# Performance work log

Hardware: AMD Instinct MI355X
Metric: run time of the kernel (lower is better)

Reference implementation:

```python
import jax, jax.numpy as jnp
import numpy as np

N_NODES = 100_000
N_EDGES = 1_600_000
N_GRAPHS = 512
D_IN = 128
D_H = 64
D_OUT = 32
N_CONV = 4  # n_layers - 1
BN_EPS = 1e-5


def setup_inputs() -> dict:
    key = jax.random.key(0)
    ks = jax.random.split(key, 10)
    h = jax.random.normal(ks[0], (N_NODES, D_IN), dtype=jnp.float32)
    src = jax.random.randint(ks[1], (N_EDGES,), 0, N_NODES, dtype=jnp.int32)
    dst = jax.random.randint(ks[2], (N_EDGES,), 0, N_NODES, dtype=jnp.int32)
    graph_ids = jnp.sort(jax.random.randint(ks[3], (N_NODES,), 0, N_GRAPHS, dtype=jnp.int32))
    s = 0.05
    fc1_w0 = jax.random.normal(ks[4], (D_IN, D_H), dtype=jnp.float32) * s
    fc1_w = jax.random.normal(ks[5], (N_CONV - 1, D_H, D_H), dtype=jnp.float32) * s
    fc2_w = jax.random.normal(ks[6], (N_CONV, D_H, D_H), dtype=jnp.float32) * s
    bn1_g = jnp.ones((N_CONV, D_H), dtype=jnp.float32)
    bn1_b = jnp.zeros((N_CONV, D_H), dtype=jnp.float32)
    bn2_g = jnp.ones((N_CONV, D_H), dtype=jnp.float32)
    bn2_b = jnp.zeros((N_CONV, D_H), dtype=jnp.float32)
    pred_w = jax.random.normal(ks[7], (N_CONV, D_H, D_OUT), dtype=jnp.float32) * s
    pred_b = jnp.zeros((N_CONV, D_OUT), dtype=jnp.float32)
    return {"h": h, "src": src, "dst": dst, "graph_ids": graph_ids,
            "fc1_w0": fc1_w0, "fc1_w": fc1_w, "fc2_w": fc2_w,
            "bn1_g": bn1_g, "bn1_b": bn1_b, "bn2_g": bn2_g, "bn2_b": bn2_b,
            "pred_w": pred_w, "pred_b": pred_b}


def _batch_norm(x, g, b):
    # PyTorch training-mode BN: batch mean, biased variance
    m = jnp.mean(x, axis=0)
    v = jnp.var(x, axis=0)
    return (x - m) * jax.lax.rsqrt(v + BN_EPS) * g + b


def reference(h, src, dst, graph_ids, fc1_w0, fc1_w, fc2_w,
              bn1_g, bn1_b, bn2_g, bn2_b, pred_w, pred_b):
    # GIN: h' = MLP((1+eps)*h + sum_{j in N(i)} h_j), eps=0 (learn_eps=False)
    score = jnp.zeros((N_GRAPHS, D_OUT), dtype=h.dtype)
    for l in range(N_CONV):
        agg = h + jax.ops.segment_sum(h[src], dst, num_segments=N_NODES)
        w1 = fc1_w0 if l == 0 else fc1_w[l - 1]
        # _MLP: fc2(relu(BN(fc1(x))))
        h = jax.nn.relu(_batch_norm(agg @ w1, bn1_g[l], bn1_b[l])) @ fc2_w[l]
        # outer BN + relu
        h = jax.nn.relu(_batch_norm(h, bn2_g[l], bn2_b[l]))
        # SumPooling per graph; readout skips layer-0 input rep, dropout is eval-mode identity
        pooled = jax.ops.segment_sum(h, graph_ids, num_segments=N_GRAPHS)
        score = score + pooled @ pred_w[l] + pred_b[l]
    return score
```

## Files before the change

### kernel.cpp

```cpp
#include <hip/hip_runtime.h>

#define N_NODES 100000
#define N_EDGES 1600000
#define N_GRAPHS 512
#define D_IN 128
#define D_H 64
#define D_OUT 32
#define N_CONV 4
#define BN_EPS 1e-5f
#define NSLOT 32

#define NB 512
#define NPB 196
#define NBUSED 511
#define CHUNK 8192
#define MAXE 4096
#define AGG_BLOCKS 2048
#define AGG_CHUNKS 3125

typedef unsigned short ushort_t;
typedef unsigned int uint_t;
typedef __attribute__((ext_vector_type(8))) short bf16x8;
typedef __attribute__((ext_vector_type(4))) float f32x4;
union U4B8 { uint4 u; bf16x8 v; };

__device__ inline float b2f(ushort_t u) {
    union { uint_t i; float f; } c; c.i = ((uint_t)u) << 16; return c.f;
}
__device__ inline ushort_t f2b(float f) {
    union { uint_t i; float f; } c; c.f = f;
    uint_t r = (c.i + 0x7fffu + ((c.i >> 16) & 1u)) >> 16;
    return (ushort_t)r;
}
__device__ inline float blo(uint_t v) { return b2f((ushort_t)(v & 0xffffu)); }
__device__ inline float bhi(uint_t v) { return b2f((ushort_t)(v >> 16)); }

__global__ __launch_bounds__(256) void zero_kernel(int* __restrict__ p, int nwords) {
    int i = blockIdx.x * 256 + threadIdx.x;
    if (i < nwords) p[i] = 0;
}

__global__ __launch_bounds__(256) void bucket_count(const int* __restrict__ dst,
                                                    int* __restrict__ bucketCnt) {
    __shared__ int l[NB];
    int t = threadIdx.x;
    for (int i = t; i < NB; i += 256) l[i] = 0;
    __syncthreads();
    long base = (long)blockIdx.x * 4096;
    for (int i = t; i < 4096; i += 256) {
        long e = base + i;
        if (e < N_EDGES) atomicAdd(&l[(unsigned)dst[e] / NPB], 1);
    }
    __syncthreads();
    for (int i = t; i < NB; i += 256) if (l[i]) atomicAdd(&bucketCnt[i], l[i]);
}

__global__ __launch_bounds__(512) void bucket_scan(const int* __restrict__ bucketCnt,
                                                   int* __restrict__ bucketOffs,
                                                   int* __restrict__ bucketCur) {
    __shared__ int s[512];
    int t = threadIdx.x;
    int v = bucketCnt[t];
    s[t] = v;
    __syncthreads();
    for (int off = 1; off < 512; off <<= 1) {
        int u = (t >= off) ? s[t - off] : 0;
        __syncthreads();
        s[t] += u;
        __syncthreads();
    }
    int excl = s[t] - v;
    bucketOffs[t] = excl;
    bucketCur[t] = excl;
    if (t == 511) bucketOffs[512] = s[511];
}

__global__ __launch_bounds__(256) void binned_scatter(const int* __restrict__ src,
                                                      const int* __restrict__ dst,
                                                      int* __restrict__ bucketCur,
                                                      uint_t* __restrict__ pairs) {
    __shared__ uint_t sortedp[CHUNK];
    __shared__ ushort_t sbkt[CHUNK];
    __shared__ int lcnt[NB], loffs[NB], lcur[NB], gbase[NB];
    __shared__ int ps[256];
    int t = threadIdx.x;
    long e0 = (long)blockIdx.x * CHUNK;
    int nvalid = (int)min((long)CHUNK, (long)N_EDGES - e0);
    for (int i = t; i < NB; i += 256) lcnt[i] = 0;
    __syncthreads();
    for (int i = t; i < nvalid; i += 256)
        atomicAdd(&lcnt[(unsigned)dst[e0 + i] / NPB], 1);
    __syncthreads();
    int a0 = lcnt[2 * t], a1 = lcnt[2 * t + 1];
    ps[t] = a0 + a1;
    __syncthreads();
    for (int off = 1; off < 256; off <<= 1) {
        int u = (t >= off) ? ps[t - off] : 0;
        __syncthreads();
        ps[t] += u;
        __syncthreads();
    }
    int ex = ps[t] - (a0 + a1);
    loffs[2 * t] = ex; loffs[2 * t + 1] = ex + a0;
    lcur[2 * t] = ex;  lcur[2 * t + 1] = ex + a0;
    __syncthreads();
    for (int i = t; i < NB; i += 256) {
        int c = lcnt[i];
        gbase[i] = c ? atomicAdd(&bucketCur[i], c) : 0;
    }
    for (int i = t; i < nvalid; i += 256) {
        int d = dst[e0 + i];
        int b = (unsigned)d / NPB;
        int pos = atomicAdd(&lcur[b], 1);
        sortedp[pos] = ((uint_t)src[e0 + i] << 9) | (uint_t)(d - b * NPB);
        sbkt[pos] = (ushort_t)b;
    }
    __syncthreads();
    for (int i = t; i < nvalid; i += 256) {
        int b = sbkt[i];
        long gpos = (long)gbase[b] + (i - loffs[b]);
        pairs[gpos] = sortedp[i];
    }
}

__global__ __launch_bounds__(256) void csr_finalize(const uint_t* __restrict__ pairs,
                                                    const int* __restrict__ bucketOffs,
                                                    int* __restrict__ offs,
                                                    int* __restrict__ csr) {
    __shared__ uint_t lp[MAXE];
    __shared__ int lsrc[MAXE];
    __shared__ int lcnt[NPB], lcur[NPB];
    __shared__ int ls[256];
    int b = blockIdx.x, t = threadIdx.x;
    int e0 = bucketOffs[b], e1 = bucketOffs[b + 1];
    int ne = e1 - e0;
    int n0 = b * NPB;
    int nn = min(NPB, N_NODES - n0);
    for (int i = t; i < ne; i += 256) lp[i] = pairs[e0 + i];
    for (int i = t; i < nn; i += 256) lcnt[i] = 0;
    __syncthreads();
    for (int i = t; i < ne; i += 256) atomicAdd(&lcnt[lp[i] & 511u], 1);
    __syncthreads();
    int v = (t < nn) ? lcnt[t] : 0;
    ls[t] = v;
    __syncthreads();
    for (int off = 1; off < 256; off <<= 1) {
        int u = (t >= off) ? ls[t - off] : 0;
        __syncthreads();
        ls[t] += u;
        __syncthreads();
    }
    if (t < nn) { lcur[t] = ls[t] - v; offs[n0 + t] = e0 + ls[t] - v; }
    if (t == 0 && b == NBUSED - 1) offs[N_NODES] = e1;
    __syncthreads();
    for (int i = t; i < ne; i += 256) {
        uint_t p = lp[i];
        int pos = atomicAdd(&lcur[p & 511u], 1);
        lsrc[pos] = (int)(p >> 9);
    }
    __syncthreads();
    for (int i = t; i < ne; i += 256) csr[e0 + i] = lsrc[i];
}

#define SLABS 4
#define GEMM_BLOCKS 391
__global__ __launch_bounds__(256) void gemm0(const float* __restrict__ in,
                                             const float* __restrict__ w,
                                             ushort_t* __restrict__ y16) {
    __shared__ uint4 Bl[4][4][64];
    int t = threadIdx.x;
    for (int idx = t; idx < 4 * 4 * 64; idx += 256) {
        int l = idx & 63, nt = (idx >> 6) & 3, kk = idx >> 8;
        int k0 = kk * 32 + ((l >> 4) << 3), c = nt * 16 + (l & 15);
        uint4 o;
        o.x = (uint_t)f2b(w[(k0 + 0) * 64 + c]) | ((uint_t)f2b(w[(k0 + 1) * 64 + c]) << 16);
        o.y = (uint_t)f2b(w[(k0 + 2) * 64 + c]) | ((uint_t)f2b(w[(k0 + 3) * 64 + c]) << 16);
        o.z = (uint_t)f2b(w[(k0 + 4) * 64 + c]) | ((uint_t)f2b(w[(k0 + 5) * 64 + c]) << 16);
        o.w = (uint_t)f2b(w[(k0 + 6) * 64 + c]) | ((uint_t)f2b(w[(k0 + 7) * 64 + c]) << 16);
        Bl[kk][nt][l] = o;
    }
    __syncthreads();
    int wv = t >> 6, lane = t & 63, lq = lane >> 4, lr = lane & 15;
    bf16x8 B[4][4];
#pragma unroll
    for (int kk = 0; kk < 4; kk++)
#pragma unroll
        for (int nt = 0; nt < 4; nt++) { U4B8 cv; cv.u = Bl[kk][nt][lane]; B[kk][nt] = cv.v; }
    for (int s = 0; s < SLABS; s++) {
        long rb = ((long)blockIdx.x * SLABS + s) * 64 + wv * 16;
        long n = rb + lr;
        const float* rp = in + (n < N_NODES ? n : 0) * 128;
        f32x4 zero = {0.f, 0.f, 0.f, 0.f};
        f32x4 acc[4] = {zero, zero, zero, zero};
#pragma unroll
        for (int kk = 0; kk < 4; kk++) {
            float4 u = *(const float4*)(rp + kk * 32 + lq * 8);
            float4 v = *(const float4*)(rp + kk * 32 + lq * 8 + 4);
            bf16x8 a;
            a[0] = (short)f2b(u.x); a[1] = (short)f2b(u.y);
            a[2] = (short)f2b(u.z); a[3] = (short)f2b(u.w);
            a[4] = (short)f2b(v.x); a[5] = (short)f2b(v.y);
            a[6] = (short)f2b(v.z); a[7] = (short)f2b(v.w);
#pragma unroll
            for (int nt = 0; nt < 4; nt++)
                acc[nt] = __builtin_amdgcn_mfma_f32_16x16x32_bf16(a, B[kk][nt], acc[nt], 0, 0, 0);
        }
#pragma unroll
        for (int nt = 0; nt < 4; nt++)
#pragma unroll
            for (int j = 0; j < 4; j++) {
                long rr = rb + lq * 4 + j;
                if (rr < N_NODES) y16[rr * 64 + nt * 16 + lr] = f2b(acc[nt][j]);
            }
    }
}

template <bool OSTAT>
__global__ __launch_bounds__(256) void gemm_bn(const uint4* __restrict__ in,
                                               const float* __restrict__ w,
                                               const float* __restrict__ bnip,
                                               const float* __restrict__ gi,
                                               const float* __restrict__ bi,
                                               ushort_t* __restrict__ outY,
                                               float* __restrict__ ostat) {
    __shared__ uint4 Bl[2][4][64];
    __shared__ float sc[64], sh[64];
    __shared__ float red1[4][64], red2[4][64];
    int t = threadIdx.x;
    if (t < 64) {
        float S = 0.f, S2 = 0.f;
        for (int s = 0; s < NSLOT; s++) { S += bnip[s * 128 + t]; S2 += bnip[s * 128 + 64 + t]; }
        float mean = S * (1.f / N_NODES);
        float var = S2 * (1.f / N_NODES) - mean * mean;
        float r = rsqrtf(var + BN_EPS);
        float scv = gi[t] * r;
        sc[t] = scv; sh[t] = bi[t] - mean * scv;
    }
    for (int idx = t; idx < 2 * 4 * 64; idx += 256) {
        int l = idx & 63, nt = (idx >> 6) & 3, kk = idx >> 8;
        int k0 = kk * 32 + ((l >> 4) << 3), c = nt * 16 + (l & 15);
        uint4 o;
        o.x = (uint_t)f2b(w[(k0 + 0) * 64 + c]) | ((uint_t)f2b(w[(k0 + 1) * 64 + c]) << 16);
        o.y = (uint_t)f2b(w[(k0 + 2) * 64 + c]) | ((uint_t)f2b(w[(k0 + 3) * 64 + c]) << 16);
        o.z = (uint_t)f2b(w[(k0 + 4) * 64 + c]) | ((uint_t)f2b(w[(k0 + 5) * 64 + c]) << 16);
        o.w = (uint_t)f2b(w[(k0 + 6) * 64 + c]) | ((uint_t)f2b(w[(k0 + 7) * 64 + c]) << 16);
        Bl[kk][nt][l] = o;
    }
    __syncthreads();
    int wv = t >> 6, lane = t & 63, lq = lane >> 4, lr = lane & 15;
    bf16x8 B[2][4];
#pragma unroll
    for (int kk = 0; kk < 2; kk++)
#pragma unroll
        for (int nt = 0; nt < 4; nt++) { U4B8 cv; cv.u = Bl[kk][nt][lane]; B[kk][nt] = cv.v; }
    float s1[4] = {0.f, 0.f, 0.f, 0.f}, s2[4] = {0.f, 0.f, 0.f, 0.f};
    for (int s = 0; s < SLABS; s++) {
        long rb = ((long)blockIdx.x * SLABS + s) * 64 + wv * 16;
        long n = rb + lr;
        bool ok = n < N_NODES;
        const uint4* rp = in + (ok ? n : 0) * 8;
        f32x4 zero = {0.f, 0.f, 0.f, 0.f};
        f32x4 acc[4] = {zero, zero, zero, zero};
#pragma unroll
        for (int kk = 0; kk < 2; kk++) {
            bf16x8 a;
            if (ok) {
                uint4 v = rp[kk * 4 + lq];
                int k0 = kk * 32 + lq * 8;
                float x0 = fmaxf(blo(v.x) * sc[k0 + 0] + sh[k0 + 0], 0.f);
                float x1 = fmaxf(bhi(v.x) * sc[k0 + 1] + sh[k0 + 1], 0.f);
                float x2 = fmaxf(blo(v.y) * sc[k0 + 2] + sh[k0 + 2], 0.f);
                float x3 = fmaxf(bhi(v.y) * sc[k0 + 3] + sh[k0 + 3], 0.f);
                float x4 = fmaxf(blo(v.z) * sc[k0 + 4] + sh[k0 + 4], 0.f);
                float x5 = fmaxf(bhi(v.z) * sc[k0 + 5] + sh[k0 + 5], 0.f);
                float x6 = fmaxf(blo(v.w) * sc[k0 + 6] + sh[k0 + 6], 0.f);
                float x7 = fmaxf(bhi(v.w) * sc[k0 + 7] + sh[k0 + 7], 0.f);
                a[0] = (short)f2b(x0); a[1] = (short)f2b(x1);
                a[2] = (short)f2b(x2); a[3] = (short)f2b(x3);
                a[4] = (short)f2b(x4); a[5] = (short)f2b(x5);
                a[6] = (short)f2b(x6); a[7] = (short)f2b(x7);
            } else {
#pragma unroll
                for (int j = 0; j < 8; j++) a[j] = 0;
            }
#pragma unroll
            for (int nt = 0; nt < 4; nt++)
                acc[nt] = __builtin_amdgcn_mfma_f32_16x16x32_bf16(a, B[kk][nt], acc[nt], 0, 0, 0);
        }
#pragma unroll
        for (int nt = 0; nt < 4; nt++)
#pragma unroll
            for (int j = 0; j < 4; j++) {
                long rr = rb + lq * 4 + j;
                float val = acc[nt][j];
                if (rr < N_NODES) outY[rr * 64 + nt * 16 + lr] = f2b(val);
                if (OSTAT) { s1[nt] += val; s2[nt] += val * val; }
            }
    }
    if (OSTAT) {
#pragma unroll
        for (int nt = 0; nt < 4; nt++) {
            s1[nt] += __shfl_xor(s1[nt], 16); s1[nt] += __shfl_xor(s1[nt], 32);
            s2[nt] += __shfl_xor(s2[nt], 16); s2[nt] += __shfl_xor(s2[nt], 32);
        }
        if (lq == 0) {
#pragma unroll
            for (int nt = 0; nt < 4; nt++) {
                red1[wv][nt * 16 + lr] = s1[nt];
                red2[wv][nt * 16 + lr] = s2[nt];
            }
        }
        __syncthreads();
        if (t < 64) {
            float S = red1[0][t] + red1[1][t] + red1[2][t] + red1[3][t];
            float S2 = red2[0][t] + red2[1][t] + red2[2][t] + red2[3][t];
            int slot = blockIdx.x & (NSLOT - 1);
            atomicAdd(&ostat[slot * 128 + t], S);
            atomicAdd(&ostat[slot * 128 + 64 + t], S2);
        }
    }
}

__global__ __launch_bounds__(256) void aggregate(const uint_t* __restrict__ y32,
                                                 const int* __restrict__ offs,
                                                 const int* __restrict__ csr,
                                                 uint_t* __restrict__ aggOut,
                                                 float* __restrict__ bn1p) {
    int t = threadIdx.x;
    int wv = t >> 6, lane = t & 63;
    int g = lane >> 3, l = lane & 7;
    __shared__ float l1[4][64], l2[4][64];
    float st1[8], st2[8];
#pragma unroll
    for (int m = 0; m < 8; m++) { st1[m] = 0.f; st2[m] = 0.f; }
    for (int chunk = blockIdx.x; chunk < AGG_CHUNKS; chunk += AGG_BLOCKS) {
        int nb_base = chunk * 32 + wv * 8;
        for (int j = 0; j < 8; j++) {
            int n = nb_base + j;
            int p0 = offs[n], p1 = offs[n + 1];
            int cnt = 1 + (p1 - p0);
            int rounds = (cnt + 7) >> 3;
            float accA[4] = {0.f, 0.f, 0.f, 0.f}, accB[4] = {0.f, 0.f, 0.f, 0.f};
            int e = g;
            int idx = (g == 0) ? n : ((g < cnt) ? csr[p0 + g - 1] : -1);
            uint4 v;
            if (idx >= 0) v = *(const uint4*)(y32 + (long)idx * 32 + 4 * l);
            for (int r = 0; r < rounds; r++) {
                int ne = e + 8;
                int nidx = (ne < cnt) ? csr[p0 + ne - 1] : -1;
                uint4 vn;
                if (nidx >= 0) vn = *(const uint4*)(y32 + (long)nidx * 32 + 4 * l);
                if (idx >= 0) {
                    accA[0] += __uint_as_float(v.x << 16);
                    accB[0] += __uint_as_float(v.x & 0xffff0000u);
                    accA[1] += __uint_as_float(v.y << 16);
                    accB[1] += __uint_as_float(v.y & 0xffff0000u);
                    accA[2] += __uint_as_float(v.z << 16);
                    accB[2] += __uint_as_float(v.z & 0xffff0000u);
                    accA[3] += __uint_as_float(v.w << 16);
                    accB[3] += __uint_as_float(v.w & 0xffff0000u);
                }
                e = ne; idx = nidx; v = vn;
            }
#pragma unroll
            for (int m = 0; m < 4; m++) {
                accA[m] += __shfl_xor(accA[m], 8);
                accB[m] += __shfl_xor(accB[m], 8);
                accA[m] += __shfl_xor(accA[m], 16);
                accB[m] += __shfl_xor(accB[m], 16);
                accA[m] += __shfl_xor(accA[m], 32);
                accB[m] += __shfl_xor(accB[m], 32);
            }
            if (g == 0) {
                uint4 o;
                o.x = (uint_t)f2b(accA[0]) | ((uint_t)f2b(accB[0]) << 16);
                o.y = (uint_t)f2b(accA[1]) | ((uint_t)f2b(accB[1]) << 16);
                o.z = (uint_t)f2b(accA[2]) | ((uint_t)f2b(accB[2]) << 16);
                o.w = (uint_t)f2b(accA[3]) | ((uint_t)f2b(accB[3]) << 16);
                *(uint4*)&aggOut[(long)n * 32 + 4 * l] = o;
                st1[0] += accA[0]; st2[0] += accA[0] * accA[0];
                st1[1] += accB[0]; st2[1] += accB[0] * accB[0];
                st1[2] += accA[1]; st2[2] += accA[1] * accA[1];
                st1[3] += accB[1]; st2[3] += accB[1] * accB[1];
                st1[4] += accA[2]; st2[4] += accA[2] * accA[2];
                st1[5] += accB[2]; st2[5] += accB[2] * accB[2];
                st1[6] += accA[3]; st2[6] += accA[3] * accA[3];
                st1[7] += accB[3]; st2[7] += accB[3] * accB[3];
            }
        }
    }
    if (g == 0) {
#pragma unroll
        for (int m = 0; m < 8; m++) { l1[wv][8 * l + m] = st1[m]; l2[wv][8 * l + m] = st2[m]; }
    }
    __syncthreads();
    if (t < 64) {
        float S = l1[0][t] + l1[1][t] + l1[2][t] + l1[3][t];
        float S2 = l2[0][t] + l2[1][t] + l2[2][t] + l2[3][t];
        int slot = blockIdx.x & (NSLOT - 1);
        atomicAdd(&bn1p[slot * 128 + t], S);
        atomicAdd(&bn1p[slot * 128 + 64 + t], S2);
    }
}

__global__ __launch_bounds__(256) void bn_pool(const uint_t* __restrict__ h2,
                                               const float* __restrict__ bn2p,
                                               const float* __restrict__ g2,
                                               const float* __restrict__ b2,
                                               const int* __restrict__ gid,
                                               float* __restrict__ pooled) {
    __shared__ float sc[64], sh[64];
    int t = threadIdx.x;
    if (t < 64) {
        float S = 0.f, S2 = 0.f;
        for (int s = 0; s < NSLOT; s++) { S += bn2p[s * 128 + t]; S2 += bn2p[s * 128 + 64 + t]; }
        float mean = S * (1.f / N_NODES);
        float var = S2 * (1.f / N_NODES) - mean * mean;
        float r = rsqrtf(var + BN_EPS);
        float scv = g2[t] * r;
        sc[t] = scv; sh[t] = b2[t] - mean * scv;
    }
    __syncthreads();
    int c = t & 31, rs = t >> 5;
    float sA = sc[2 * c], hA = sh[2 * c], sB = sc[2 * c + 1], hB = sh[2 * c + 1];
    long base = (long)blockIdx.x * 256;
    float pa = 0.f, pb2 = 0.f; int gc = -1;
    for (int i = 0; i < 32; i++) {
        long n = base + rs + 8 * i;
        if (n >= N_NODES) break;
        int g = gid[n];
        uint_t v = h2[n * 32 + c];
        float x0 = fmaxf(blo(v) * sA + hA, 0.f);
        float x1 = fmaxf(bhi(v) * sB + hB, 0.f);
        if (g != gc) {
            if (gc >= 0) {
                atomicAdd(&pooled[(long)gc * 64 + 2 * c], pa);
                atomicAdd(&pooled[(long)gc * 64 + 2 * c + 1], pb2);
            }
            gc = g; pa = 0.f; pb2 = 0.f;
        }
        pa += x0; pb2 += x1;
    }
    if (gc >= 0) {
        atomicAdd(&pooled[(long)gc * 64 + 2 * c], pa);
        atomicAdd(&pooled[(long)gc * 64 + 2 * c + 1], pb2);
    }
}

__global__ __launch_bounds__(256) void score_kernel(const float* __restrict__ pooled,
                                                    const float* __restrict__ pw,
                                                    const float* __restrict__ pb,
                                                    float* __restrict__ out) {
    int idx = blockIdx.x * 256 + threadIdx.x;
    int g = idx >> 5, o = idx & 31;
    float acc = 0.f;
    for (int l = 0; l < N_CONV; l++) {
        acc += pb[l * 32 + o];
        const float* pr = pooled + (long)l * N_GRAPHS * 64 + (long)g * 64;
        const float* wr = pw + l * 64 * 32;
        for (int k = 0; k < 64; k++) acc += pr[k] * wr[k * 32 + o];
    }
    out[idx] = acc;
}

extern "C" void kernel_launch(void* const* d_in, const int* in_sizes, int n_in,
                              void* d_out, int out_size, void* d_ws, size_t ws_size,
                              hipStream_t stream) {
    const float* h     = (const float*)d_in[0];
    const int*   src   = (const int*)d_in[1];
    const int*   dst   = (const int*)d_in[2];
    const int*   gid   = (const int*)d_in[3];
    const float* fc1w0 = (const float*)d_in[4];
    const float* fc1w  = (const float*)d_in[5];
    const float* fc2w  = (const float*)d_in[6];
    const float* bn1g  = (const float*)d_in[7];
    const float* bn1b  = (const float*)d_in[8];
    const float* bn2g  = (const float*)d_in[9];
    const float* bn2b  = (const float*)d_in[10];
    const float* pw    = (const float*)d_in[11];
    const float* pb    = (const float*)d_in[12];
    float* out = (float*)d_out;

    char* ws = (char*)d_ws;
    uint_t*   AGG16   = (uint_t*)  (ws);
    uint_t*   pairs   = (uint_t*)  (ws);
    ushort_t* X16     = (ushort_t*)(ws + 25600000);
    ushort_t* Y16     = (ushort_t*)(ws + 38400000);
    float*    bnst    = (float*)   (ws + 51200000);
    float*    pooled  = (float*)   (ws + 51331072);
    int*   bucketCnt  = (int*)     (ws + 51855360);
    int*   bucketOffs = (int*)     (ws + 51857408);
    int*   bucketCur  = (int*)     (ws + 51859460);
    int*   offs       = (int*)     (ws + 51861508);
    int*   csr        = (int*)     (ws + 52261512);

    const int zwords = (51857408 - 51200000) / 4;
    zero_kernel<<<(zwords + 255) / 256, 256, 0, stream>>>((int*)bnst, zwords);

    bucket_count<<<(N_EDGES + 4095) / 4096, 256, 0, stream>>>(dst, bucketCnt);
    bucket_scan<<<1, 512, 0, stream>>>(bucketCnt, bucketOffs, bucketCur);
    binned_scatter<<<(N_EDGES + CHUNK - 1) / CHUNK, 256, 0, stream>>>(src, dst, bucketCur, pairs);
    csr_finalize<<<NBUSED, 256, 0, stream>>>(pairs, bucketOffs, offs, csr);

    for (int l = 0; l < N_CONV; l++) {
        float* bn1p = bnst + (long)l * 8192;
        float* bn2p = bn1p + 4096;
        float* pl = pooled + (long)l * N_GRAPHS * 64;
        if (l == 0) {
            gemm0<<<GEMM_BLOCKS, 256, 0, stream>>>(h, fc1w0, Y16);
        } else {
            float* bn2p_prev = bnst + (long)(l - 1) * 8192 + 4096;
            gemm_bn<false><<<GEMM_BLOCKS, 256, 0, stream>>>((const uint4*)X16,
                fc1w + (long)(l - 1) * 4096, bn2p_prev,
                bn2g + (l - 1) * 64, bn2b + (l - 1) * 64, Y16, (float*)nullptr);
        }
        aggregate<<<AGG_BLOCKS, 256, 0, stream>>>((const uint_t*)Y16, offs, csr, AGG16, bn1p);
        gemm_bn<true><<<GEMM_BLOCKS, 256, 0, stream>>>((const uint4*)AGG16,
            fc2w + (long)l * 4096, bn1p, bn1g + l * 64, bn1b + l * 64, X16, bn2p);
        bn_pool<<<391, 256, 0, stream>>>((const uint_t*)X16, bn2p, bn2g + l * 64,
                                         bn2b + l * 64, gid, pl);
    }
    score_kernel<<<64, 256, 0, stream>>>(pooled, pw, pb, out);
}
```

Before: 405.7 us.

## Pipeline neighbor gathers via async global-to-LDS loads and shrink GEMM block work

The aggregate kernel now prefetches each node's first few neighbor rows straight into shared memory with global_load_lds, double-buffered two nodes ahead, and falls back to direct loads for high-degree nodes. This is meant to hide the gather latency that the old per-round register prefetch left exposed. The GEMM kernels also get more blocks with fewer row slabs each, for better occupancy. The cost is higher LDS use and hand-written waitcnt values that must match the number of outstanding loads.

Measured after the change: 420.9 us. 1.04x slower.

```diff
diff --git a/kernel.cpp b/kernel.cpp
--- a/kernel.cpp
+++ b/kernel.cpp
@@ -17,12 +17,16 @@
 #define MAXE 4096
 #define AGG_BLOCKS 2048
 #define AGG_CHUNKS 3125
+#define R_STAT 3
 
 typedef unsigned short ushort_t;
 typedef unsigned int uint_t;
 typedef __attribute__((ext_vector_type(8))) short bf16x8;
 typedef __attribute__((ext_vector_type(4))) float f32x4;
 union U4B8 { uint4 u; bf16x8 v; };
+
+typedef const __attribute__((address_space(1))) uint_t guint_t;
+typedef __attribute__((address_space(3))) uint_t luint_t;
 
 __device__ inline float b2f(ushort_t u) {
     union { uint_t i; float f; } c; c.i = ((uint_t)u) << 16; return c.f;
@@ -162,8 +166,9 @@
     for (int i = t; i < ne; i += 256) csr[e0 + i] = lsrc[i];
 }
 
-#define SLABS 4
-#define GEMM_BLOCKS 391
+#define G0_SLABS 2
+#define G0_BLOCKS 782
+#define GBN_BLOCKS 1563
 __global__ __launch_bounds__(256) void gemm0(const float* __restrict__ in,
                                              const float* __restrict__ w,
                                              ushort_t* __restrict__ y16) {
@@ -186,8 +191,8 @@
     for (int kk = 0; kk < 4; kk++)
 #pragma unroll
         for (int nt = 0; nt < 4; nt++) { U4B8 cv; cv.u = Bl[kk][nt][lane]; B[kk][nt] = cv.v; }
-    for (int s = 0; s < SLABS; s++) {
-        long rb = ((long)blockIdx.x * SLABS + s) * 64 + wv * 16;
+    for (int s = 0; s < G0_SLABS; s++) {
+        long rb = ((long)blockIdx.x * G0_SLABS + s) * 64 + wv * 16;
         long n = rb + lr;
         const float* rp = in + (n < N_NODES ? n : 0) * 128;
         f32x4 zero = {0.f, 0.f, 0.f, 0.f};
@@ -254,49 +259,48 @@
 #pragma unroll
         for (int nt = 0; nt < 4; nt++) { U4B8 cv; cv.u = Bl[kk][nt][lane]; B[kk][nt] = cv.v; }
     float s1[4] = {0.f, 0.f, 0.f, 0.f}, s2[4] = {0.f, 0.f, 0.f, 0.f};
-    for (int s = 0; s < SLABS; s++) {
-        long rb = ((long)blockIdx.x * SLABS + s) * 64 + wv * 16;
-        long n = rb + lr;
-        bool ok = n < N_NODES;
-        const uint4* rp = in + (ok ? n : 0) * 8;
-        f32x4 zero = {0.f, 0.f, 0.f, 0.f};
-        f32x4 acc[4] = {zero, zero, zero, zero};
-#pragma unroll
-        for (int kk = 0; kk < 2; kk++) {
-            bf16x8 a;
-            if (ok) {
-                uint4 v = rp[kk * 4 + lq];
-                int k0 = kk * 32 + lq * 8;
-                float x0 = fmaxf(blo(v.x) * sc[k0 + 0] + sh[k0 + 0], 0.f);
-                float x1 = fmaxf(bhi(v.x) * sc[k0 + 1] + sh[k0 + 1], 0.f);
-                float x2 = fmaxf(blo(v.y) * sc[k0 + 2] + sh[k0 + 2], 0.f);
-                float x3 = fmaxf(bhi(v.y) * sc[k0 + 3] + sh[k0 + 3], 0.f);
-                float x4 = fmaxf(blo(v.z) * sc[k0 + 4] + sh[k0 + 4], 0.f);
-                float x5 = fmaxf(bhi(v.z) * sc[k0 + 5] + sh[k0 + 5], 0.f);
-                float x6 = fmaxf(blo(v.w) * sc[k0 + 6] + sh[k0 + 6], 0.f);
-                float x7 = fmaxf(bhi(v.w) * sc[k0 + 7] + sh[k0 + 7], 0.f);
-                a[0] = (short)f2b(x0); a[1] = (short)f2b(x1);
-                a[2] = (short)f2b(x2); a[3] = (short)f2b(x3);
-                a[4] = (short)f2b(x4); a[5] = (short)f2b(x5);
-                a[6] = (short)f2b(x6); a[7] = (short)f2b(x7);
-            } else {
-#pragma unroll
-                for (int j = 0; j < 8; j++) a[j] = 0;
-            }
-#pragma unroll
-            for (int nt = 0; nt < 4; nt++)
-                acc[nt] = __builtin_amdgcn_mfma_f32_16x16x32_bf16(a, B[kk][nt], acc[nt], 0, 0, 0);
+    long rb = (long)blockIdx.x * 64 + wv * 16;
+    long n = rb + lr;
+    bool ok = n < N_NODES;
+    const uint4* rp = in + (ok ? n : 0) * 8;
+    f32x4 zero = {0.f, 0.f, 0.f, 0.f};
+    f32x4 acc[4] = {zero, zero, zero, zero};
+#pragma unroll
+    for (int kk = 0; kk < 2; kk++) {
+        bf16x8 a;
+        if (ok) {
+            uint4 v = rp[kk * 4 + lq];
+            int k0 = kk * 32 + lq * 8;
+            float x0 = fmaxf(blo(v.x) * sc[k0 + 0] + sh[k0 + 0], 0.f);
+            float x1 = fmaxf(bhi(v.x) * sc[k0 + 1] + sh[k0 + 1], 0.f);
+            float x2 = fmaxf(blo(v.y) * sc[k0 + 2] + sh[k0 + 2], 0.f);
+            float x3 = fmaxf(bhi(v.y) * sc[k0 + 3] + sh[k0 + 3], 0.f);
+            float x4 = fmaxf(blo(v.z) * sc[k0 + 4] + sh[k0 + 4], 0.f);
+            float x5 = fmaxf(bhi(v.z) * sc[k0 + 5] + sh[k0 + 5], 0.f);
+            float x6 = fmaxf(blo(v.w) * sc[k0 + 6] + sh[k0 + 6], 0.f);
+            float x7 = fmaxf(bhi(v.w) * sc[k0 + 7] + sh[k0 + 7], 0.f);
+            a[0] = (short)f2b(x0); a[1] = (short)f2b(x1);
+            a[2] = (short)f2b(x2); a[3] = (short)f2b(x3);
+            a[4] = (short)f2b(x4); a[5] = (short)f2b(x5);
+            a[6] = (short)f2b(x6); a[7] = (short)f2b(x7);
+        } else {
+#pragma unroll
+            for (int j = 0; j < 8; j++) a[j] = 0;
         }
 #pragma unroll
         for (int nt = 0; nt < 4; nt++)
-#pragma unroll
-            for (int j = 0; j < 4; j++) {
-                long rr = rb + lq * 4 + j;
-                float val = acc[nt][j];
-                if (rr < N_NODES) outY[rr * 64 + nt * 16 + lr] = f2b(val);
-                if (OSTAT) { s1[nt] += val; s2[nt] += val * val; }
-            }
-    }
+            acc[nt] = __builtin_amdgcn_mfma_f32_16x16x32_bf16(a, B[kk][nt], acc[nt], 0, 0, 0);
+    }
+#pragma unroll
+    for (int nt = 0; nt < 4; nt++)
+#pragma unroll
+        for (int j = 0; j < 4; j++) {
+            long rr = rb + lq * 4 + j;
+            float val = acc[nt][j];
+            if (rr < N_NODES) outY[rr * 64 + nt * 16 + lr] = f2b(val);
+            else val = 0.f;
+            if (OSTAT) { s1[nt] += val; s2[nt] += val * val; }
+        }
     if (OSTAT) {
 #pragma unroll
         for (int nt = 0; nt < 4; nt++) {
@@ -326,31 +330,64 @@
                                                  const int* __restrict__ csr,
                                                  uint_t* __restrict__ aggOut,
                                                  float* __restrict__ bn1p) {
+    __shared__ uint4 stage[4][2][R_STAT][64];
+    __shared__ float l1[4][64], l2[4][64];
     int t = threadIdx.x;
     int wv = t >> 6, lane = t & 63;
     int g = lane >> 3, l = lane & 7;
-    __shared__ float l1[4][64], l2[4][64];
     float st1[8], st2[8];
 #pragma unroll
     for (int m = 0; m < 8; m++) { st1[m] = 0.f; st2[m] = 0.f; }
     for (int chunk = blockIdx.x; chunk < AGG_CHUNKS; chunk += AGG_BLOCKS) {
-        int nb_base = chunk * 32 + wv * 8;
+        int nb = chunk * 32 + wv * 8;
+        int offv = offs[nb + (lane < 9 ? lane : 8)];
+        int p0c = __shfl(offv, 0);
+        int cntc = __shfl(offv, 1) - p0c + 1;
+        int idxN[R_STAT], idxF[R_STAT];
+        {
+            int idx0[R_STAT];
+#pragma unroll
+            for (int r = 0; r < R_STAT; r++) {
+                int e = r * 8 + g;
+                idx0[r] = (e == 0) ? nb : ((e < cntc) ? csr[p0c + e - 1] : nb);
+            }
+#pragma unroll
+            for (int r = 0; r < R_STAT; r++)
+                __builtin_amdgcn_global_load_lds(
+                    (guint_t*)(y32 + (long)idx0[r] * 32 + 4 * l),
+                    (luint_t*)&stage[wv][0][r][0], 16, 0, 0);
+        }
+        int p0n = __shfl(offv, 1);
+        int cntn = __shfl(offv, 2) - p0n + 1;
+#pragma unroll
+        for (int r = 0; r < R_STAT; r++) {
+            int e = r * 8 + g;
+            idxN[r] = (e == 0) ? (nb + 1) : ((e < cntn) ? csr[p0n + e - 1] : (nb + 1));
+        }
+#pragma unroll 1
         for (int j = 0; j < 8; j++) {
-            int n = nb_base + j;
-            int p0 = offs[n], p1 = offs[n + 1];
-            int cnt = 1 + (p1 - p0);
-            int rounds = (cnt + 7) >> 3;
+            int p = j & 1, pn = p ^ 1;
+            int j2 = (j + 2 < 8) ? (j + 2) : 7;
+            int p0f = __shfl(offv, j2);
+            int cntf = __shfl(offv, j2 + 1) - p0f + 1;
+#pragma unroll
+            for (int r = 0; r < R_STAT; r++) {
+                int e = r * 8 + g;
+                idxF[r] = (e == 0) ? (nb + j2) : ((e < cntf) ? csr[p0f + e - 1] : (nb + j2));
+            }
+#pragma unroll
+            for (int r = 0; r < R_STAT; r++)
+                __builtin_amdgcn_global_load_lds(
+                    (guint_t*)(y32 + (long)idxN[r] * 32 + 4 * l),
+                    (luint_t*)&stage[wv][pn][r][0], 16, 0, 0);
+            asm volatile("s_waitcnt vmcnt(6)" ::: "memory");
+            __builtin_amdgcn_sched_barrier(0);
+            int n = nb + j;
             float accA[4] = {0.f, 0.f, 0.f, 0.f}, accB[4] = {0.f, 0.f, 0.f, 0.f};
-            int e = g;
-            int idx = (g == 0) ? n : ((g < cnt) ? csr[p0 + g - 1] : -1);
-            uint4 v;
-            if (idx >= 0) v = *(const uint4*)(y32 + (long)idx * 32 + 4 * l);
-            for (int r = 0; r < rounds; r++) {
-                int ne = e + 8;
-                int nidx = (ne < cnt) ? csr[p0 + ne - 1] : -1;
-                uint4 vn;
-                if (nidx >= 0) vn = *(const uint4*)(y32 + (long)nidx * 32 + 4 * l);
-                if (idx >= 0) {
+#pragma unroll
+            for (int r = 0; r < R_STAT; r++) {
+                uint4 v = stage[wv][p][r][lane];
+                if (r * 8 + g < cntc) {
                     accA[0] += __uint_as_float(v.x << 16);
                     accB[0] += __uint_as_float(v.x & 0xffff0000u);
                     accA[1] += __uint_as_float(v.y << 16);
@@ -360,7 +397,20 @@
                     accA[3] += __uint_as_float(v.w << 16);
                     accB[3] += __uint_as_float(v.w & 0xffff0000u);
                 }
-                e = ne; idx = nidx; v = vn;
+            }
+            if (cntc > 8 * R_STAT) {
+                for (int e = 8 * R_STAT + g; e < cntc; e += 8) {
+                    int idx = csr[p0c + e - 1];
+                    uint4 v = *(const uint4*)(y32 + (long)idx * 32 + 4 * l);
+                    accA[0] += __uint_as_float(v.x << 16);
+                    accB[0] += __uint_as_float(v.x & 0xffff0000u);
+                    accA[1] += __uint_as_float(v.y << 16);
+                    accB[1] += __uint_as_float(v.y & 0xffff0000u);
+                    accA[2] += __uint_as_float(v.z << 16);
+                    accB[2] += __uint_as_float(v.z & 0xffff0000u);
+                    accA[3] += __uint_as_float(v.w << 16);
+                    accB[3] += __uint_as_float(v.w & 0xffff0000u);
+                }
             }
 #pragma unroll
             for (int m = 0; m < 4; m++) {
@@ -387,6 +437,10 @@
                 st1[6] += accA[3]; st2[6] += accA[3] * accA[3];
                 st1[7] += accB[3]; st2[7] += accB[3] * accB[3];
             }
+            p0c = p0n; cntc = cntn;
+            p0n = p0f; cntn = cntf;
+#pragma unroll
+            for (int r = 0; r < R_STAT; r++) idxN[r] = idxF[r];
         }
     }
     if (g == 0) {
@@ -507,15 +561,15 @@
         float* bn2p = bn1p + 4096;
         float* pl = pooled + (long)l * N_GRAPHS * 64;
         if (l == 0) {
-            gemm0<<<GEMM_BLOCKS, 256, 0, stream>>>(h, fc1w0, Y16);
+            gemm0<<<G0_BLOCKS, 256, 0, stream>>>(h, fc1w0, Y16);
         } else {
             float* bn2p_prev = bnst + (long)(l - 1) * 8192 + 4096;
-            gemm_bn<false><<<GEMM_BLOCKS, 256, 0, stream>>>((const uint4*)X16,
+            gemm_bn<false><<<GBN_BLOCKS, 256, 0, stream>>>((const uint4*)X16,
                 fc1w + (long)(l - 1) * 4096, bn2p_prev,
                 bn2g + (l - 1) * 64, bn2b + (l - 1) * 64, Y16, (float*)nullptr);
         }
         aggregate<<<AGG_BLOCKS, 256, 0, stream>>>((const uint_t*)Y16, offs, csr, AGG16, bn1p);
-        gemm_bn<true><<<GEMM_BLOCKS, 256, 0, stream>>>((const uint4*)AGG16,
+        gemm_bn<true><<<GBN_BLOCKS, 256, 0, stream>>>((const uint4*)AGG16,
             fc2w + (long)l * 4096, bn1p, bn1g + l * 64, bn1b + l * 64, X16, bn2p);
         bn_pool<<<391, 256, 0, stream>>>((const uint_t*)X16, bn2p, bn2g + l * 64,
                                          bn2b + l * 64, gid, pl);
```

## Store gather features in column-quarter planes and split aggregation by quarter

Applied to the files above, without the earlier changes.

The pre-aggregation feature matrix Y16 is now written by both GEMMs as four column planes of 16 bf16 values (32 bytes per node per plane). The aggregate kernel assigns each block one quarter, so a block's gathers touch a 3.2 MB plane that fits better in cache, and each node's neighbours are gathered by 2 lanes instead of 8. The GEMM kernels drop the per-block slab loop in favour of more blocks, and the gather loop no longer prefetches the next row, which could expose more latency. The edge lists are now read four times, once per quarter.

Result: no change. 411.6 us (+1.5%).

```diff
diff --git a/kernel.cpp b/kernel.cpp
--- a/kernel.cpp
+++ b/kernel.cpp
@@ -162,8 +162,9 @@
     for (int i = t; i < ne; i += 256) csr[e0 + i] = lsrc[i];
 }
 
-#define SLABS 4
-#define GEMM_BLOCKS 391
+#define G0_SLABS 2
+#define G0_BLOCKS 782
+#define GBN_BLOCKS 1563
 __global__ __launch_bounds__(256) void gemm0(const float* __restrict__ in,
                                              const float* __restrict__ w,
                                              ushort_t* __restrict__ y16) {
@@ -186,8 +187,8 @@
     for (int kk = 0; kk < 4; kk++)
 #pragma unroll
         for (int nt = 0; nt < 4; nt++) { U4B8 cv; cv.u = Bl[kk][nt][lane]; B[kk][nt] = cv.v; }
-    for (int s = 0; s < SLABS; s++) {
-        long rb = ((long)blockIdx.x * SLABS + s) * 64 + wv * 16;
+    for (int s = 0; s < G0_SLABS; s++) {
+        long rb = ((long)blockIdx.x * G0_SLABS + s) * 64 + wv * 16;
         long n = rb + lr;
         const float* rp = in + (n < N_NODES ? n : 0) * 128;
         f32x4 zero = {0.f, 0.f, 0.f, 0.f};
@@ -210,7 +211,8 @@
 #pragma unroll
             for (int j = 0; j < 4; j++) {
                 long rr = rb + lq * 4 + j;
-                if (rr < N_NODES) y16[rr * 64 + nt * 16 + lr] = f2b(acc[nt][j]);
+                if (rr < N_NODES)
+                    y16[((long)nt * N_NODES + rr) * 16 + lr] = f2b(acc[nt][j]);
             }
     }
 }
@@ -254,49 +256,50 @@
 #pragma unroll
         for (int nt = 0; nt < 4; nt++) { U4B8 cv; cv.u = Bl[kk][nt][lane]; B[kk][nt] = cv.v; }
     float s1[4] = {0.f, 0.f, 0.f, 0.f}, s2[4] = {0.f, 0.f, 0.f, 0.f};
-    for (int s = 0; s < SLABS; s++) {
-        long rb = ((long)blockIdx.x * SLABS + s) * 64 + wv * 16;
-        long n = rb + lr;
-        bool ok = n < N_NODES;
-        const uint4* rp = in + (ok ? n : 0) * 8;
-        f32x4 zero = {0.f, 0.f, 0.f, 0.f};
-        f32x4 acc[4] = {zero, zero, zero, zero};
-#pragma unroll
-        for (int kk = 0; kk < 2; kk++) {
-            bf16x8 a;
-            if (ok) {
-                uint4 v = rp[kk * 4 + lq];
-                int k0 = kk * 32 + lq * 8;
-                float x0 = fmaxf(blo(v.x) * sc[k0 + 0] + sh[k0 + 0], 0.f);
-                float x1 = fmaxf(bhi(v.x) * sc[k0 + 1] + sh[k0 + 1], 0.f);
-                float x2 = fmaxf(blo(v.y) * sc[k0 + 2] + sh[k0 + 2], 0.f);
-                float x3 = fmaxf(bhi(v.y) * sc[k0 + 3] + sh[k0 + 3], 0.f);
-                float x4 = fmaxf(blo(v.z) * sc[k0 + 4] + sh[k0 + 4], 0.f);
-                float x5 = fmaxf(bhi(v.z) * sc[k0 + 5] + sh[k0 + 5], 0.f);
-                float x6 = fmaxf(blo(v.w) * sc[k0 + 6] + sh[k0 + 6], 0.f);
-                float x7 = fmaxf(bhi(v.w) * sc[k0 + 7] + sh[k0 + 7], 0.f);
-                a[0] = (short)f2b(x0); a[1] = (short)f2b(x1);
-                a[2] = (short)f2b(x2); a[3] = (short)f2b(x3);
-                a[4] = (short)f2b(x4); a[5] = (short)f2b(x5);
-                a[6] = (short)f2b(x6); a[7] = (short)f2b(x7);
-            } else {
-#pragma unroll
-                for (int j = 0; j < 8; j++) a[j] = 0;
-            }
-#pragma unroll
-            for (int nt = 0; nt < 4; nt++)
-                acc[nt] = __builtin_amdgcn_mfma_f32_16x16x32_bf16(a, B[kk][nt], acc[nt], 0, 0, 0);
+    long rb = (long)blockIdx.x * 64 + wv * 16;
+    long n = rb + lr;
+    bool ok = n < N_NODES;
+    const uint4* rp = in + (ok ? n : 0) * 8;
+    f32x4 zero = {0.f, 0.f, 0.f, 0.f};
+    f32x4 acc[4] = {zero, zero, zero, zero};
+#pragma unroll
+    for (int kk = 0; kk < 2; kk++) {
+        bf16x8 a;
+        if (ok) {
+            uint4 v = rp[kk * 4 + lq];
+            int k0 = kk * 32 + lq * 8;
+            float x0 = fmaxf(blo(v.x) * sc[k0 + 0] + sh[k0 + 0], 0.f);
+            float x1 = fmaxf(bhi(v.x) * sc[k0 + 1] + sh[k0 + 1], 0.f);
+            float x2 = fmaxf(blo(v.y) * sc[k0 + 2] + sh[k0 + 2], 0.f);
+            float x3 = fmaxf(bhi(v.y) * sc[k0 + 3] + sh[k0 + 3], 0.f);
+            float x4 = fmaxf(blo(v.z) * sc[k0 + 4] + sh[k0 + 4], 0.f);
+            float x5 = fmaxf(bhi(v.z) * sc[k0 + 5] + sh[k0 + 5], 0.f);
+            float x6 = fmaxf(blo(v.w) * sc[k0 + 6] + sh[k0 + 6], 0.f);
+            float x7 = fmaxf(bhi(v.w) * sc[k0 + 7] + sh[k0 + 7], 0.f);
+            a[0] = (short)f2b(x0); a[1] = (short)f2b(x1);
+            a[2] = (short)f2b(x2); a[3] = (short)f2b(x3);
+            a[4] = (short)f2b(x4); a[5] = (short)f2b(x5);
+            a[6] = (short)f2b(x6); a[7] = (short)f2b(x7);
+        } else {
+#pragma unroll
+            for (int j = 0; j < 8; j++) a[j] = 0;
         }
 #pragma unroll
         for (int nt = 0; nt < 4; nt++)
-#pragma unroll
-            for (int j = 0; j < 4; j++) {
-                long rr = rb + lq * 4 + j;
-                float val = acc[nt][j];
-                if (rr < N_NODES) outY[rr * 64 + nt * 16 + lr] = f2b(val);
-                if (OSTAT) { s1[nt] += val; s2[nt] += val * val; }
-            }
-    }
+            acc[nt] = __builtin_amdgcn_mfma_f32_16x16x32_bf16(a, B[kk][nt], acc[nt], 0, 0, 0);
+    }
+#pragma unroll
+    for (int nt = 0; nt < 4; nt++)
+#pragma unroll
+        for (int j = 0; j < 4; j++) {
+            long rr = rb + lq * 4 + j;
+            float val = acc[nt][j];
+            if (rr < N_NODES) {
+                if (OSTAT) outY[rr * 64 + nt * 16 + lr] = f2b(val);
+                else       outY[((long)nt * N_NODES + rr) * 16 + lr] = f2b(val);
+            } else val = 0.f;
+            if (OSTAT) { s1[nt] += val; s2[nt] += val * val; }
+        }
     if (OSTAT) {
 #pragma unroll
         for (int nt = 0; nt < 4; nt++) {
@@ -328,29 +331,27 @@
                                                  float* __restrict__ bn1p) {
     int t = threadIdx.x;
     int wv = t >> 6, lane = t & 63;
-    int g = lane >> 3, l = lane & 7;
+    int g = lane >> 3, jj = (lane >> 1) & 3, h = lane & 1;
+    int q = blockIdx.x & 3;
+    const uint_t* yq = y32 + (long)q * N_NODES * 8;
     __shared__ float l1[4][64], l2[4][64];
     float st1[8], st2[8];
 #pragma unroll
     for (int m = 0; m < 8; m++) { st1[m] = 0.f; st2[m] = 0.f; }
-    for (int chunk = blockIdx.x; chunk < AGG_CHUNKS; chunk += AGG_BLOCKS) {
-        int nb_base = chunk * 32 + wv * 8;
-        for (int j = 0; j < 8; j++) {
-            int n = nb_base + j;
-            int p0 = offs[n], p1 = offs[n + 1];
-            int cnt = 1 + (p1 - p0);
-            int rounds = (cnt + 7) >> 3;
+    for (int c = (blockIdx.x >> 2); c < AGG_CHUNKS; c += AGG_BLOCKS / 4) {
+        int nb = c * 32 + wv * 8;
+        for (int grp = 0; grp < 2; grp++) {
+            int n = nb + grp * 4 + jj;
+            int p0 = offs[n];
+            int cnt = offs[n + 1] - p0 + 1;
             float accA[4] = {0.f, 0.f, 0.f, 0.f}, accB[4] = {0.f, 0.f, 0.f, 0.f};
             int e = g;
-            int idx = (g == 0) ? n : ((g < cnt) ? csr[p0 + g - 1] : -1);
-            uint4 v;
-            if (idx >= 0) v = *(const uint4*)(y32 + (long)idx * 32 + 4 * l);
-            for (int r = 0; r < rounds; r++) {
+            int idx = (e == 0) ? n : ((e < cnt) ? csr[p0 + e - 1] : -1);
+            while (__any(idx >= 0)) {
                 int ne = e + 8;
                 int nidx = (ne < cnt) ? csr[p0 + ne - 1] : -1;
-                uint4 vn;
-                if (nidx >= 0) vn = *(const uint4*)(y32 + (long)nidx * 32 + 4 * l);
                 if (idx >= 0) {
+                    uint4 v = *(const uint4*)(yq + (long)idx * 8 + h * 4);
                     accA[0] += __uint_as_float(v.x << 16);
                     accB[0] += __uint_as_float(v.x & 0xffff0000u);
                     accA[1] += __uint_as_float(v.y << 16);
@@ -360,7 +361,7 @@
                     accA[3] += __uint_as_float(v.w << 16);
                     accB[3] += __uint_as_float(v.w & 0xffff0000u);
                 }
-                e = ne; idx = nidx; v = vn;
+                e = ne; idx = nidx;
             }
 #pragma unroll
             for (int m = 0; m < 4; m++) {
@@ -377,7 +378,7 @@
                 o.y = (uint_t)f2b(accA[1]) | ((uint_t)f2b(accB[1]) << 16);
                 o.z = (uint_t)f2b(accA[2]) | ((uint_t)f2b(accB[2]) << 16);
                 o.w = (uint_t)f2b(accA[3]) | ((uint_t)f2b(accB[3]) << 16);
-                *(uint4*)&aggOut[(long)n * 32 + 4 * l] = o;
+                *(uint4*)&aggOut[(long)n * 32 + q * 8 + h * 4] = o;
                 st1[0] += accA[0]; st2[0] += accA[0] * accA[0];
                 st1[1] += accB[0]; st2[1] += accB[0] * accB[0];
                 st1[2] += accA[1]; st2[2] += accA[1] * accA[1];
@@ -391,15 +392,24 @@
     }
     if (g == 0) {
 #pragma unroll
-        for (int m = 0; m < 8; m++) { l1[wv][8 * l + m] = st1[m]; l2[wv][8 * l + m] = st2[m]; }
-    }
-    __syncthreads();
-    if (t < 64) {
-        float S = l1[0][t] + l1[1][t] + l1[2][t] + l1[3][t];
-        float S2 = l2[0][t] + l2[1][t] + l2[2][t] + l2[3][t];
+        for (int m = 0; m < 8; m++) {
+            l1[wv][jj * 16 + h * 8 + m] = st1[m];
+            l2[wv][jj * 16 + h * 8 + m] = st2[m];
+        }
+    }
+    __syncthreads();
+    if (t < 16) {
+        float S = 0.f, S2 = 0.f;
+#pragma unroll
+        for (int w = 0; w < 4; w++)
+#pragma unroll
+            for (int j2 = 0; j2 < 4; j2++) {
+                S += l1[w][j2 * 16 + t];
+                S2 += l2[w][j2 * 16 + t];
+            }
         int slot = blockIdx.x & (NSLOT - 1);
-        atomicAdd(&bn1p[slot * 128 + t], S);
-        atomicAdd(&bn1p[slot * 128 + 64 + t], S2);
+        atomicAdd(&bn1p[slot * 128 + q * 16 + t], S);
+        atomicAdd(&bn1p[slot * 128 + 64 + q * 16 + t], S2);
     }
 }
 
@@ -507,15 +517,15 @@
         float* bn2p = bn1p + 4096;
         float* pl = pooled + (long)l * N_GRAPHS * 64;
         if (l == 0) {
-            gemm0<<<GEMM_BLOCKS, 256, 0, stream>>>(h, fc1w0, Y16);
+            gemm0<<<G0_BLOCKS, 256, 0, stream>>>(h, fc1w0, Y16);
         } else {
             float* bn2p_prev = bnst + (long)(l - 1) * 8192 + 4096;
-            gemm_bn<false><<<GEMM_BLOCKS, 256, 0, stream>>>((const uint4*)X16,
+            gemm_bn<false><<<GBN_BLOCKS, 256, 0, stream>>>((const uint4*)X16,
                 fc1w + (long)(l - 1) * 4096, bn2p_prev,
                 bn2g + (l - 1) * 64, bn2b + (l - 1) * 64, Y16, (float*)nullptr);
         }
         aggregate<<<AGG_BLOCKS, 256, 0, stream>>>((const uint_t*)Y16, offs, csr, AGG16, bn1p);
-        gemm_bn<true><<<GEMM_BLOCKS, 256, 0, stream>>>((const uint4*)AGG16,
+        gemm_bn<true><<<GBN_BLOCKS, 256, 0, stream>>>((const uint4*)AGG16,
             fc2w + (long)l * 4096, bn1p, bn1g + l * 64, bn1b + l * 64, X16, bn2p);
         bn_pool<<<391, 256, 0, stream>>>((const uint_t*)X16, bn2p, bn2g + l * 64,
                                          bn2b + l * 64, gid, pl);
```
